# Kernel optimization log

Measured on AMD Instinct MI355X. Metric: run time of the kernel, lower is better.

The kernel has to match this reference:

```python
import jax, jax.numpy as jnp
import numpy as np

B, D, P, K_ROUTE = 131072, 256, 16, 4


def setup_inputs() -> dict:
    key = jax.random.key(0)
    ks = jax.random.split(key, 12)
    w_scale = 0.02
    return {
        "z_n": jax.random.normal(ks[0], (B, D), dtype=jnp.float32),
        "z_sea": jax.random.normal(ks[1], (B, D), dtype=jnp.float32),
        "z_trend": jax.random.normal(ks[2], (B, D), dtype=jnp.float32),
        "noise_z": jax.random.normal(ks[3], (B, D), dtype=jnp.float32),   # randn_like(z_fused)
        "noise_r": jax.random.normal(ks[4], (B, P), dtype=jnp.float32),   # randn_like(routing_logits)
        "patch_candidates": jax.random.randint(ks[5], (P,), 1, 64, dtype=jnp.int32),
        "W_proj": jax.random.normal(ks[6], (D, 3 * D), dtype=jnp.float32) * w_scale,
        "b_proj": jnp.zeros((D,), dtype=jnp.float32),
        "W_route": jax.random.normal(ks[7], (P, D), dtype=jnp.float32) * w_scale,
        "b_route": jnp.zeros((P,), dtype=jnp.float32),
        "W_noise": jax.random.normal(ks[8], (P, D), dtype=jnp.float32) * w_scale,
        "b_noise": jnp.zeros((P,), dtype=jnp.float32),
    }


def reference(z_n, z_sea, z_trend, noise_z, noise_r, patch_candidates,
              W_proj, b_proj, W_route, b_route, W_noise, b_noise):
    # feature fusion: Linear(3D -> D) on concat
    z_concat = jnp.concatenate([z_n, z_sea, z_trend], axis=-1)        # [B, 3D]
    z_fused = z_concat @ W_proj.T + b_proj                            # [B, D]
    gating_input = z_fused + noise_z * 0.1                            # noise injection 1
    routing_logits = gating_input @ W_route.T + b_route               # [B, P]
    noise_scale = jax.nn.softplus(gating_input @ W_noise.T + b_noise)  # [B, P]
    routing_logits = routing_logits + noise_r * noise_scale           # noise injection 2
    routing_weights = jax.nn.softmax(routing_logits, axis=-1)         # [B, P]
    top_k_values, top_k_indices = jax.lax.top_k(routing_weights, K_ROUTE)  # [B, K]
    rows = jnp.arange(routing_weights.shape[0])[:, None]
    sparse_routing = jnp.zeros_like(routing_weights).at[rows, top_k_indices].set(top_k_values)
    selected_patches = patch_candidates[top_k_indices]                # [B, K]
    return (sparse_routing, selected_patches, top_k_indices)
```

## Files before the change

kernel.cpp:

```cpp
#include <hip/hip_runtime.h>
#include <math.h>

#define B_ROWS 131072
#define ROWS 128
#define XP 36
#define MP 36
#define LP 34

__global__ void precompute_M(const float* __restrict__ Wp,
                             const float* __restrict__ Wr,
                             const float* __restrict__ Wn,
                             const float* __restrict__ bp,
                             const float* __restrict__ br,
                             const float* __restrict__ bn,
                             float* __restrict__ M,
                             float* __restrict__ c) {
  int o = blockIdx.x * 256 + threadIdx.x;
  if (o < 32 * 1024) {
    int j = o >> 10, k = o & 1023;
    const float* W = (j < 16) ? Wr : Wn;
    int jj = j & 15;
    float v;
    if (k < 768) {
      double s0 = 0.0, s1 = 0.0, s2 = 0.0, s3 = 0.0;
      for (int d = 0; d < 256; d += 4) {
        s0 += (double)W[jj * 256 + d]     * (double)Wp[(d)     * 768 + k];
        s1 += (double)W[jj * 256 + d + 1] * (double)Wp[(d + 1) * 768 + k];
        s2 += (double)W[jj * 256 + d + 2] * (double)Wp[(d + 2) * 768 + k];
        s3 += (double)W[jj * 256 + d + 3] * (double)Wp[(d + 3) * 768 + k];
      }
      v = (float)((s0 + s1) + (s2 + s3));
    } else {
      v = 0.1f * W[jj * 256 + (k - 768)];
    }
    M[o] = v;
  }
  if (blockIdx.x == 0 && threadIdx.x < 32) {
    int j = threadIdx.x, jj = j & 15;
    const float* W = (j < 16) ? Wr : Wn;
    const float* b = (j < 16) ? br : bn;
    double s = (double)b[jj];
    for (int d = 0; d < 256; ++d)
      s += (double)W[jj * 256 + d] * (double)bp[d];
    c[j] = (float)s;
  }
}

#define LOAD_STAGE(S_) do {                                                   \
    const int k0_ = (S_) * 32;                                                \
    const float* src_; int col0_;                                             \
    if (k0_ < 256)      { src_ = zn; col0_ = k0_; }                           \
    else if (k0_ < 512) { src_ = zs; col0_ = k0_ - 256; }                     \
    else if (k0_ < 768) { src_ = zt; col0_ = k0_ - 512; }                     \
    else                { src_ = nz; col0_ = k0_ - 768; }                     \
    const float* base_ = src_ + (size_t)(row0 + sr) * 256 + col0_ + 4 * sk4;  \
    xg0 = *(const float4*)(base_);                                            \
    xg1 = *(const float4*)(base_ + 32 * 256);                                 \
    xg2 = *(const float4*)(base_ + 64 * 256);                                 \
    xg3 = *(const float4*)(base_ + 96 * 256);                                 \
    mg  = *(const float4*)&M[(size_t)sr * 1024 + k0_ + 4 * sk4];              \
  } while (0)

__global__ __launch_bounds__(256, 3)
void router_main(const float* __restrict__ zn, const float* __restrict__ zs,
                 const float* __restrict__ zt, const float* __restrict__ nz,
                 const float* __restrict__ nr, const int* __restrict__ patches,
                 const float* __restrict__ M, const float* __restrict__ c,
                 float* __restrict__ out) {
  __shared__ float Xs[ROWS * XP];
  __shared__ float Ms[32 * MP];
  float* const Ls = Xs;

  const int t = threadIdx.x;
  const int row0 = blockIdx.x * ROWS;
  const int jg = t & 7;
  const int rg = t >> 3;
  const int sr = t >> 3;
  const int sk4 = t & 7;

  float accf[4][4];
  double accd[4][4];
#pragma unroll
  for (int a = 0; a < 4; ++a)
#pragma unroll
    for (int b = 0; b < 4; ++b) { accf[a][b] = 0.f; accd[a][b] = 0.0; }

  float4 xg0, xg1, xg2, xg3, mg;

  LOAD_STAGE(0);

  for (int s = 0; s < 32; ++s) {
    __syncthreads();
    *(float4*)&Xs[(sr +  0) * XP + 4 * sk4] = xg0;
    *(float4*)&Xs[(sr + 32) * XP + 4 * sk4] = xg1;
    *(float4*)&Xs[(sr + 64) * XP + 4 * sk4] = xg2;
    *(float4*)&Xs[(sr + 96) * XP + 4 * sk4] = xg3;
    *(float4*)&Ms[sr * MP + 4 * sk4] = mg;
    __syncthreads();

    if (s < 31) LOAD_STAGE(s + 1);

#pragma unroll
    for (int ks = 0; ks < 8; ++ks) {
      const int k = 4 * ks;
      float4 m4[4], x4[4];
#pragma unroll
      for (int jj = 0; jj < 4; ++jj)
        m4[jj] = *(const float4*)&Ms[(jg + 8 * jj) * MP + k];
#pragma unroll
      for (int rr = 0; rr < 4; ++rr)
        x4[rr] = *(const float4*)&Xs[(rg + 32 * rr) * XP + k];
#pragma unroll
      for (int jj = 0; jj < 4; ++jj)
#pragma unroll
        for (int rr = 0; rr < 4; ++rr) {
          accf[jj][rr] += m4[jj].x * x4[rr].x;
          accf[jj][rr] += m4[jj].y * x4[rr].y;
          accf[jj][rr] += m4[jj].z * x4[rr].z;
          accf[jj][rr] += m4[jj].w * x4[rr].w;
        }
    }
#pragma unroll
    for (int jj = 0; jj < 4; ++jj)
#pragma unroll
      for (int rr = 0; rr < 4; ++rr) { accd[jj][rr] += (double)accf[jj][rr]; accf[jj][rr] = 0.f; }
  }

  __syncthreads();

#pragma unroll
  for (int jj = 0; jj < 4; ++jj) {
    const int j = jg + 8 * jj;
    const float cj = c[j];
#pragma unroll
    for (int rr = 0; rr < 4; ++rr) {
      const int r = rg + 32 * rr;
      Ls[r * LP + j] = (float)(accd[jj][rr] + (double)cj);
    }
  }
  __syncthreads();

  if (t < ROWS) {
    const int row = row0 + t;
    float L[32];
#pragma unroll
    for (int j = 0; j < 32; ++j) L[j] = Ls[t * LP + j];

    float nrv[16];
#pragma unroll
    for (int q = 0; q < 4; ++q) {
      float4 v = *(const float4*)&nr[(size_t)row * 16 + 4 * q];
      nrv[4 * q] = v.x; nrv[4 * q + 1] = v.y; nrv[4 * q + 2] = v.z; nrv[4 * q + 3] = v.w;
    }

    float lg[16];
#pragma unroll
    for (int p = 0; p < 16; ++p) {
      const float x = L[16 + p];
      const float sp = (x > 15.f) ? x : log1pf(expf(x));
      lg[p] = L[p] + nrv[p] * sp;
    }

    float mx = lg[0];
#pragma unroll
    for (int p = 1; p < 16; ++p) mx = fmaxf(mx, lg[p]);
    float e[16]; float sum = 0.f;
#pragma unroll
    for (int p = 0; p < 16; ++p) { e[p] = expf(lg[p] - mx); sum += e[p]; }
    float w[16];
#pragma unroll
    for (int p = 0; p < 16; ++p) w[p] = e[p] / sum;

    int idx[4]; float val[4]; unsigned used = 0;
#pragma unroll
    for (int kk = 0; kk < 4; ++kk) {
      float best = -1.f; int bi = 0;
#pragma unroll
      for (int p = 0; p < 16; ++p) {
        const bool ok = (((used >> p) & 1u) == 0u) && (w[p] > best);
        best = ok ? w[p] : best;
        bi = ok ? p : bi;
      }
      idx[kk] = bi; val[kk] = best; used |= (1u << bi);
    }

    float so[16];
#pragma unroll
    for (int p = 0; p < 16; ++p) {
      float v = 0.f;
#pragma unroll
      for (int kk = 0; kk < 4; ++kk) v = (idx[kk] == p) ? val[kk] : v;
      so[p] = v;
    }
#pragma unroll
    for (int q = 0; q < 4; ++q)
      *(float4*)&out[(size_t)row * 16 + 4 * q] =
          make_float4(so[4 * q], so[4 * q + 1], so[4 * q + 2], so[4 * q + 3]);

    float4 pv, iv;
    pv.x = (float)patches[idx[0]]; pv.y = (float)patches[idx[1]];
    pv.z = (float)patches[idx[2]]; pv.w = (float)patches[idx[3]];
    iv.x = (float)idx[0]; iv.y = (float)idx[1];
    iv.z = (float)idx[2]; iv.w = (float)idx[3];
    *(float4*)&out[(size_t)B_ROWS * 16 + (size_t)row * 4] = pv;
    *(float4*)&out[(size_t)B_ROWS * 20 + (size_t)row * 4] = iv;
  }
}

extern "C" void kernel_launch(void* const* d_in, const int* in_sizes, int n_in,
                              void* d_out, int out_size, void* d_ws, size_t ws_size,
                              hipStream_t stream) {
  const float* zn = (const float*)d_in[0];
  const float* zs = (const float*)d_in[1];
  const float* zt = (const float*)d_in[2];
  const float* nz = (const float*)d_in[3];
  const float* nr = (const float*)d_in[4];
  const int*   pc = (const int*)d_in[5];
  const float* Wp = (const float*)d_in[6];
  const float* bp = (const float*)d_in[7];
  const float* Wr = (const float*)d_in[8];
  const float* br = (const float*)d_in[9];
  const float* Wn = (const float*)d_in[10];
  const float* bn = (const float*)d_in[11];
  float* out = (float*)d_out;
  float* M = (float*)d_ws;
  float* c = M + 32 * 1024;

  precompute_M<<<128, 256, 0, stream>>>(Wp, Wr, Wn, bp, br, bn, M, c);
  router_main<<<B_ROWS / ROWS, 256, 0, stream>>>(zn, zs, zt, nz, nr, pc, M, c, out);
}
```

Before: 529.7 us.

## Replace FP32 FMA inner product with split-bf16 MFMA emulation

After: 501.3 us. 5.3% less time.

```diff
diff --git a/kernel.cpp b/kernel.cpp
--- a/kernel.cpp
+++ b/kernel.cpp
@@ -3,9 +3,22 @@
 
 #define B_ROWS 131072
 #define ROWS 128
-#define XP 36
-#define MP 36
+#define XPB 40
 #define LP 34
+
+typedef __attribute__((ext_vector_type(8))) short short8v;
+typedef __attribute__((ext_vector_type(4))) short short4v;
+typedef __attribute__((ext_vector_type(4))) float float4v;
+
+__device__ __forceinline__ short f2bf(float x) {
+  unsigned u = __builtin_bit_cast(unsigned, x);
+  u += 0x7fffu + ((u >> 16) & 1u);
+  return (short)(u >> 16);
+}
+__device__ __forceinline__ float bf2f(short h) {
+  unsigned u = ((unsigned)(unsigned short)h) << 16;
+  return __builtin_bit_cast(float, u);
+}
 
 __global__ void precompute_M(const float* __restrict__ Wp,
                              const float* __restrict__ Wr,
@@ -61,81 +74,129 @@
     mg  = *(const float4*)&M[(size_t)sr * 1024 + k0_ + 4 * sk4];              \
   } while (0)
 
+#define CVT3(VG_, PH_, PM_, PL_, OFF_) do {                                   \
+    short4v h_, m_, l_;                                                       \
+    float v_, r_;                                                             \
+    v_ = VG_.x; h_[0] = f2bf(v_); r_ = v_ - bf2f(h_[0]);                      \
+    m_[0] = f2bf(r_); l_[0] = f2bf(r_ - bf2f(m_[0]));                         \
+    v_ = VG_.y; h_[1] = f2bf(v_); r_ = v_ - bf2f(h_[1]);                      \
+    m_[1] = f2bf(r_); l_[1] = f2bf(r_ - bf2f(m_[1]));                         \
+    v_ = VG_.z; h_[2] = f2bf(v_); r_ = v_ - bf2f(h_[2]);                      \
+    m_[2] = f2bf(r_); l_[2] = f2bf(r_ - bf2f(m_[2]));                         \
+    v_ = VG_.w; h_[3] = f2bf(v_); r_ = v_ - bf2f(h_[3]);                      \
+    m_[3] = f2bf(r_); l_[3] = f2bf(r_ - bf2f(m_[3]));                         \
+    *(short4v*)&PH_[OFF_] = h_;                                               \
+    *(short4v*)&PM_[OFF_] = m_;                                               \
+    *(short4v*)&PL_[OFF_] = l_;                                               \
+  } while (0)
+
 __global__ __launch_bounds__(256, 3)
 void router_main(const float* __restrict__ zn, const float* __restrict__ zs,
                  const float* __restrict__ zt, const float* __restrict__ nz,
                  const float* __restrict__ nr, const int* __restrict__ patches,
                  const float* __restrict__ M, const float* __restrict__ c,
                  float* __restrict__ out) {
-  __shared__ float Xs[ROWS * XP];
-  __shared__ float Ms[32 * MP];
-  float* const Ls = Xs;
+  __shared__ __align__(16) char smem[38400];
+  short* const Xh  = (short*)smem;
+  short* const Xm  = (short*)(smem + 10240);
+  short* const Xl  = (short*)(smem + 20480);
+  short* const Mhs = (short*)(smem + 30720);
+  short* const Mms = (short*)(smem + 33280);
+  short* const Mls = (short*)(smem + 35840);
+  float* const Ls  = (float*)smem;
 
   const int t = threadIdx.x;
   const int row0 = blockIdx.x * ROWS;
-  const int jg = t & 7;
-  const int rg = t >> 3;
   const int sr = t >> 3;
   const int sk4 = t & 7;
-
-  float accf[4][4];
-  double accd[4][4];
-#pragma unroll
-  for (int a = 0; a < 4; ++a)
-#pragma unroll
-    for (int b = 0; b < 4; ++b) { accf[a][b] = 0.f; accd[a][b] = 0.0; }
+  const int lane = t & 63;
+  const int w = t >> 6;
+
+  float4v aB00 = {0,0,0,0}, aB01 = {0,0,0,0}, aB10 = {0,0,0,0}, aB11 = {0,0,0,0};
+  float4v aS00 = {0,0,0,0}, aS01 = {0,0,0,0}, aS10 = {0,0,0,0}, aS11 = {0,0,0,0};
+  double d00[4], d01[4], d10[4], d11[4];
+#pragma unroll
+  for (int r = 0; r < 4; ++r) { d00[r] = 0.0; d01[r] = 0.0; d10[r] = 0.0; d11[r] = 0.0; }
 
   float4 xg0, xg1, xg2, xg3, mg;
+
+  const int aoff = (w * 32 + (lane & 15)) * XPB + (lane >> 4) * 8;
+  const int boff = (lane & 15) * XPB + (lane >> 4) * 8;
+  const int soff = sr * XPB + 4 * sk4;
 
   LOAD_STAGE(0);
 
   for (int s = 0; s < 32; ++s) {
     __syncthreads();
-    *(float4*)&Xs[(sr +  0) * XP + 4 * sk4] = xg0;
-    *(float4*)&Xs[(sr + 32) * XP + 4 * sk4] = xg1;
-    *(float4*)&Xs[(sr + 64) * XP + 4 * sk4] = xg2;
-    *(float4*)&Xs[(sr + 96) * XP + 4 * sk4] = xg3;
-    *(float4*)&Ms[sr * MP + 4 * sk4] = mg;
+    CVT3(xg0, Xh, Xm, Xl, soff);
+    CVT3(xg1, Xh, Xm, Xl, soff + 32 * XPB);
+    CVT3(xg2, Xh, Xm, Xl, soff + 64 * XPB);
+    CVT3(xg3, Xh, Xm, Xl, soff + 96 * XPB);
+    CVT3(mg, Mhs, Mms, Mls, soff);
     __syncthreads();
 
     if (s < 31) LOAD_STAGE(s + 1);
 
-#pragma unroll
-    for (int ks = 0; ks < 8; ++ks) {
-      const int k = 4 * ks;
-      float4 m4[4], x4[4];
-#pragma unroll
-      for (int jj = 0; jj < 4; ++jj)
-        m4[jj] = *(const float4*)&Ms[(jg + 8 * jj) * MP + k];
-#pragma unroll
-      for (int rr = 0; rr < 4; ++rr)
-        x4[rr] = *(const float4*)&Xs[(rg + 32 * rr) * XP + k];
-#pragma unroll
-      for (int jj = 0; jj < 4; ++jj)
-#pragma unroll
-        for (int rr = 0; rr < 4; ++rr) {
-          accf[jj][rr] += m4[jj].x * x4[rr].x;
-          accf[jj][rr] += m4[jj].y * x4[rr].y;
-          accf[jj][rr] += m4[jj].z * x4[rr].z;
-          accf[jj][rr] += m4[jj].w * x4[rr].w;
-        }
-    }
-#pragma unroll
-    for (int jj = 0; jj < 4; ++jj)
-#pragma unroll
-      for (int rr = 0; rr < 4; ++rr) { accd[jj][rr] += (double)accf[jj][rr]; accf[jj][rr] = 0.f; }
+    short8v ah0 = *(const short8v*)&Xh[aoff];
+    short8v ah1 = *(const short8v*)&Xh[aoff + 16 * XPB];
+    short8v am0 = *(const short8v*)&Xm[aoff];
+    short8v am1 = *(const short8v*)&Xm[aoff + 16 * XPB];
+    short8v al0 = *(const short8v*)&Xl[aoff];
+    short8v al1 = *(const short8v*)&Xl[aoff + 16 * XPB];
+    short8v bh0 = *(const short8v*)&Mhs[boff];
+    short8v bh1 = *(const short8v*)&Mhs[boff + 16 * XPB];
+    short8v bm0 = *(const short8v*)&Mms[boff];
+    short8v bm1 = *(const short8v*)&Mms[boff + 16 * XPB];
+    short8v bl0 = *(const short8v*)&Mls[boff];
+    short8v bl1 = *(const short8v*)&Mls[boff + 16 * XPB];
+
+    aB00 = __builtin_amdgcn_mfma_f32_16x16x32_bf16(ah0, bh0, aB00, 0, 0, 0);
+    aB01 = __builtin_amdgcn_mfma_f32_16x16x32_bf16(ah0, bh1, aB01, 0, 0, 0);
+    aB10 = __builtin_amdgcn_mfma_f32_16x16x32_bf16(ah1, bh0, aB10, 0, 0, 0);
+    aB11 = __builtin_amdgcn_mfma_f32_16x16x32_bf16(ah1, bh1, aB11, 0, 0, 0);
+    aS00 = __builtin_amdgcn_mfma_f32_16x16x32_bf16(ah0, bm0, aS00, 0, 0, 0);
+    aS01 = __builtin_amdgcn_mfma_f32_16x16x32_bf16(ah0, bm1, aS01, 0, 0, 0);
+    aS10 = __builtin_amdgcn_mfma_f32_16x16x32_bf16(ah1, bm0, aS10, 0, 0, 0);
+    aS11 = __builtin_amdgcn_mfma_f32_16x16x32_bf16(ah1, bm1, aS11, 0, 0, 0);
+    aS00 = __builtin_amdgcn_mfma_f32_16x16x32_bf16(am0, bh0, aS00, 0, 0, 0);
+    aS01 = __builtin_amdgcn_mfma_f32_16x16x32_bf16(am0, bh1, aS01, 0, 0, 0);
+    aS10 = __builtin_amdgcn_mfma_f32_16x16x32_bf16(am1, bh0, aS10, 0, 0, 0);
+    aS11 = __builtin_amdgcn_mfma_f32_16x16x32_bf16(am1, bh1, aS11, 0, 0, 0);
+    aS00 = __builtin_amdgcn_mfma_f32_16x16x32_bf16(ah0, bl0, aS00, 0, 0, 0);
+    aS01 = __builtin_amdgcn_mfma_f32_16x16x32_bf16(ah0, bl1, aS01, 0, 0, 0);
+    aS10 = __builtin_amdgcn_mfma_f32_16x16x32_bf16(ah1, bl0, aS10, 0, 0, 0);
+    aS11 = __builtin_amdgcn_mfma_f32_16x16x32_bf16(ah1, bl1, aS11, 0, 0, 0);
+    aS00 = __builtin_amdgcn_mfma_f32_16x16x32_bf16(al0, bh0, aS00, 0, 0, 0);
+    aS01 = __builtin_amdgcn_mfma_f32_16x16x32_bf16(al0, bh1, aS01, 0, 0, 0);
+    aS10 = __builtin_amdgcn_mfma_f32_16x16x32_bf16(al1, bh0, aS10, 0, 0, 0);
+    aS11 = __builtin_amdgcn_mfma_f32_16x16x32_bf16(al1, bh1, aS11, 0, 0, 0);
+    aS00 = __builtin_amdgcn_mfma_f32_16x16x32_bf16(am0, bm0, aS00, 0, 0, 0);
+    aS01 = __builtin_amdgcn_mfma_f32_16x16x32_bf16(am0, bm1, aS01, 0, 0, 0);
+    aS10 = __builtin_amdgcn_mfma_f32_16x16x32_bf16(am1, bm0, aS10, 0, 0, 0);
+    aS11 = __builtin_amdgcn_mfma_f32_16x16x32_bf16(am1, bm1, aS11, 0, 0, 0);
+
+#pragma unroll
+    for (int r = 0; r < 4; ++r) {
+      d00[r] += (double)aB00[r] + (double)aS00[r]; aB00[r] = 0.f; aS00[r] = 0.f;
+      d01[r] += (double)aB01[r] + (double)aS01[r]; aB01[r] = 0.f; aS01[r] = 0.f;
+      d10[r] += (double)aB10[r] + (double)aS10[r]; aB10[r] = 0.f; aS10[r] = 0.f;
+      d11[r] += (double)aB11[r] + (double)aS11[r]; aB11[r] = 0.f; aS11[r] = 0.f;
+    }
   }
 
   __syncthreads();
 
-#pragma unroll
-  for (int jj = 0; jj < 4; ++jj) {
-    const int j = jg + 8 * jj;
-    const float cj = c[j];
-#pragma unroll
-    for (int rr = 0; rr < 4; ++rr) {
-      const int r = rg + 32 * rr;
-      Ls[r * LP + j] = (float)(accd[jj][rr] + (double)cj);
+  {
+    const double c0 = (double)c[lane & 15];
+    const double c1 = (double)c[16 + (lane & 15)];
+    const int er = w * 32 + (lane >> 4) * 4;
+    const int jc = lane & 15;
+#pragma unroll
+    for (int reg = 0; reg < 4; ++reg) {
+      Ls[(er + reg) * LP + jc]           = (float)(d00[reg] + c0);
+      Ls[(er + reg) * LP + 16 + jc]      = (float)(d01[reg] + c1);
+      Ls[(er + 16 + reg) * LP + jc]      = (float)(d10[reg] + c0);
+      Ls[(er + 16 + reg) * LP + 16 + jc] = (float)(d11[reg] + c1);
     }
   }
   __syncthreads();
@@ -167,9 +228,9 @@
     float e[16]; float sum = 0.f;
 #pragma unroll
     for (int p = 0; p < 16; ++p) { e[p] = expf(lg[p] - mx); sum += e[p]; }
-    float w[16];
-#pragma unroll
-    for (int p = 0; p < 16; ++p) w[p] = e[p] / sum;
+    float w2[16];
+#pragma unroll
+    for (int p = 0; p < 16; ++p) w2[p] = e[p] / sum;
 
     int idx[4]; float val[4]; unsigned used = 0;
 #pragma unroll
@@ -177,8 +238,8 @@
       float best = -1.f; int bi = 0;
 #pragma unroll
       for (int p = 0; p < 16; ++p) {
-        const bool ok = (((used >> p) & 1u) == 0u) && (w[p] > best);
-        best = ok ? w[p] : best;
+        const bool ok = (((used >> p) & 1u) == 0u) && (w2[p] > best);
+        best = ok ? w2[p] : best;
         bi = ok ? p : bi;
       }
       idx[kk] = bi; val[kk] = best; used |= (1u << bi);
```
